# Kernel optimization log

Measured on AMD Instinct MI355X. Metric: run time of the kernel, lower is better.

Reference implementation:

```python
import jax, jax.numpy as jnp
import numpy as np

B_, K_, C_, HID_, T_, H_, W_ = 4, 4096, 384, 1536, 8, 32, 32
L_ = T_ * H_ * W_


def setup_inputs() -> dict:
    key = jax.random.key(0)
    ks = jax.random.split(key, 8)
    x_sparse = jax.random.normal(ks[0], (B_, K_, C_), dtype=jnp.float32)
    # unique, sorted per-batch active-token indices in [0, L)
    perm_keys = jax.random.split(ks[1], B_)
    indices = jax.vmap(lambda k: jnp.sort(jax.random.permutation(k, L_)[:K_]))(perm_keys).astype(jnp.int32)
    std = 0.02
    w1 = jax.random.normal(ks[2], (HID_, C_), dtype=jnp.float32) * std
    b1 = jnp.zeros((HID_,), dtype=jnp.float32)
    dw_w = jax.random.normal(ks[3], (HID_, 1, 3, 3), dtype=jnp.float32) * std  # depthwise OIHW, I=1
    dw_b = jnp.zeros((HID_,), dtype=jnp.float32)
    w2 = jax.random.normal(ks[4], (C_, HID_), dtype=jnp.float32) * std
    b2 = jnp.zeros((C_,), dtype=jnp.float32)
    return {"x_sparse": x_sparse, "indices": indices, "B": B_, "L": L_, "H": H_, "W": W_,
            "w1": w1, "b1": b1, "dw_w": dw_w, "dw_b": dw_b, "w2": w2, "b2": b2}


def reference(x_sparse, indices, B, L, H, W, w1, b1, dw_w, dw_b, w2, b2):
    K = x_sparse.shape[1]
    HID = w1.shape[0]
    T = L // (H * W)
    # sparse fc1: [B,K,C] @ [C,HID]
    h = jnp.einsum('bkc,hc->bkh', x_sparse, w1) + b1
    # scatter active tokens into zero-initialized dense grid [B,L,HID]
    bidx = jnp.arange(B)[:, None]  # [B,1]
    dense = jnp.zeros((B, L, HID), dtype=h.dtype).at[bidx, indices].set(h)
    # dense depthwise 3x3 conv on [B*T, HID, H, W]
    xs = dense.reshape(B * T, H, W, HID).transpose(0, 3, 1, 2)
    xs = jax.lax.conv_general_dilated(
        xs, dw_w, window_strides=(1, 1), padding='SAME',
        feature_group_count=HID,
        dimension_numbers=('NCHW', 'OIHW', 'NCHW')) + dw_b[None, :, None, None]
    flat = xs.transpose(0, 2, 3, 1).reshape(B, L, HID)
    # gather back the active tokens
    g = flat[bidx, indices]  # [B,K,HID]
    g = jax.nn.gelu(g, approximate=False)  # torch nn.GELU default is exact erf
    # sparse fc2: [B,K,HID] @ [HID,C_out]
    out = jnp.einsum('bkh,ch->bkc', g, w2) + b2
    return out
```

## Files before the change

### kernel.cpp

```cpp
#include <hip/hip_runtime.h>
#include <stdint.h>

using u16 = unsigned short;
using u32 = unsigned int;
using f32x4 = __attribute__((ext_vector_type(4))) float;
using s16x8 = __attribute__((ext_vector_type(8))) short;

#define DEVINL __device__ __forceinline__

constexpr int B_ = 4, K_ = 4096, C_ = 384, HID_ = 1536, H_ = 32, W_ = 32, L_ = 8192;
constexpr int M_ = B_ * K_;

DEVINL u16 f2bf(float f) {
    u32 u = __builtin_bit_cast(u32, f);
    u32 r = (u + 0x7FFFu + ((u >> 16) & 1u)) >> 16;
    return (u16)r;
}
DEVINL float bf2f(u16 h) {
    u32 u = ((u32)h) << 16;
    return __builtin_bit_cast(float, u);
}

template <int N>
DEVINL void wait_vmcnt() {
    asm volatile("s_waitcnt vmcnt(%0)" ::"n"(N) : "memory");
}

__global__ __launch_bounds__(256) void prep_kernel(
    const float* __restrict__ x, const float* __restrict__ w1, const float* __restrict__ w2,
    const float* __restrict__ dww, const int* __restrict__ indices,
    u16* __restrict__ xb, u16* __restrict__ w1b, u16* __restrict__ w2b,
    float* __restrict__ dwT, int* __restrict__ pos2k, u16* __restrict__ hzero) {
    const int i = blockIdx.x * 256 + threadIdx.x;
    if (i < 933888) {
        const float* src;
        u16* dst;
        if (i < 786432) { src = x + (size_t)i * 8; dst = xb + (size_t)i * 8; }
        else if (i < 860160) { src = w1 + (size_t)(i - 786432) * 8; dst = w1b + (size_t)(i - 786432) * 8; }
        else { src = w2 + (size_t)(i - 860160) * 8; dst = w2b + (size_t)(i - 860160) * 8; }
        float4 a = ((const float4*)src)[0];
        float4 b = ((const float4*)src)[1];
        s16x8 o;
        o[0] = (short)f2bf(a.x); o[1] = (short)f2bf(a.y);
        o[2] = (short)f2bf(a.z); o[3] = (short)f2bf(a.w);
        o[4] = (short)f2bf(b.x); o[5] = (short)f2bf(b.y);
        o[6] = (short)f2bf(b.z); o[7] = (short)f2bf(b.w);
        *(s16x8*)dst = o;
    } else if (i < 947712) {
        int t = i - 933888;
        int j = t / 1536;
        int hh = t - j * 1536;
        dwT[j * 1536 + hh] = dww[hh * 9 + j];
    } else if (i < 964096) {
        int t = i - 947712;
        int b = t >> 12;
        pos2k[(b << 13) + indices[t]] = t & 4095;
    } else if (i < 964288) {
        int t = i - 964096;
        s16x8 z = {0, 0, 0, 0, 0, 0, 0, 0};
        *(s16x8*)(hzero + t * 8) = z;
    }
}

template <int BM, int BN, int KDIM, bool OUT_BF16, int CB, int DEPTH>
__global__ __launch_bounds__(256) void gemm_pipe_kernel(
    const u16* __restrict__ A,
    const u16* __restrict__ Bt,
    const float* __restrict__ bias,
    void* __restrict__ Cv,
    int Ndim) {
    constexpr int BK = 32;
    constexpr int NSTEPS = KDIM / BK;
    static_assert(NSTEPS >= DEPTH, "");
    static_assert(DEPTH == 3 || DEPTH == 4, "");
    constexpr int ACH = BM / 16;
    constexpr int BCH = BN / 16;
    constexpr int CPW = (ACH + BCH) / 4;
    constexpr int ASZ = BM * BK;
    constexpr int BSZ = BN * BK;
    constexpr int FM = BM / 32;
    constexpr int FN = BN / 32;
    __shared__ u16 As[DEPTH * ASZ];
    __shared__ u16 Bs[DEPTH * BSZ];

    const int flat = blockIdx.x;
    const int per = gridDim.x >> 3;
    const int lid = (flat & 7) * per + (flat >> 3);
    const int rb = lid / CB;
    const int cb = lid - rb * CB;
    const int row0 = rb * BM;
    const int col0 = cb * BN;

    const int tid = threadIdx.x;
    const int wave = tid >> 6;
    const int lane = tid & 63;
    const int sr = lane >> 2;
    const int scw = (((lane & 3) ^ ((sr >> 1) & 3))) * 8;
    const int wr = (wave >> 1) * (FM * 16);
    const int wc = (wave & 1) * (FN * 16);
    const int fq = lane >> 4;
    const int fr = lane & 15;
    const int rchunk = fq ^ ((fr >> 1) & 3);

    f32x4 acc[FM][FN];
#pragma unroll
    for (int m = 0; m < FM; ++m)
#pragma unroll
        for (int n = 0; n < FN; ++n) acc[m][n] = f32x4{0.f, 0.f, 0.f, 0.f};

    const int c0ch = wave * CPW;

    auto stage = [&](int bi, int k0) {
#pragma unroll
        for (int q = 0; q < CPW; ++q) {
            const int c = c0ch + q;
            if (c < ACH) {
                const u16* g = A + (size_t)(row0 + c * 16 + sr) * KDIM + k0 + scw;
                __builtin_amdgcn_global_load_lds(
                    (const __attribute__((address_space(1))) void*)g,
                    (__attribute__((address_space(3))) void*)(As + bi * ASZ + c * 512), 16, 0, 0);
            } else {
                const int cc = c - ACH;
                const u16* g = Bt + (size_t)(col0 + cc * 16 + sr) * KDIM + k0 + scw;
                __builtin_amdgcn_global_load_lds(
                    (const __attribute__((address_space(1))) void*)g,
                    (__attribute__((address_space(3))) void*)(Bs + bi * BSZ + cc * 512), 16, 0, 0);
            }
        }
    };

    auto compute = [&](int bi) {
        s16x8 af[FM], bf_[FN];
#pragma unroll
        for (int m = 0; m < FM; ++m)
            af[m] = *(const s16x8*)(As + bi * ASZ + (wr + m * 16 + fr) * BK + rchunk * 8);
#pragma unroll
        for (int n = 0; n < FN; ++n)
            bf_[n] = *(const s16x8*)(Bs + bi * BSZ + (wc + n * 16 + fr) * BK + rchunk * 8);
        __builtin_amdgcn_s_setprio(1);
#pragma unroll
        for (int m = 0; m < FM; ++m)
#pragma unroll
            for (int n = 0; n < FN; ++n)
                acc[m][n] = __builtin_amdgcn_mfma_f32_16x16x32_bf16(af[m], bf_[n], acc[m][n], 0, 0, 0);
        __builtin_amdgcn_s_setprio(0);
    };

#pragma unroll
    for (int p = 0; p < DEPTH - 1; ++p) stage(p, p * BK);

    for (int i = 0; i < NSTEPS - (DEPTH - 1); ++i) {
        wait_vmcnt<(DEPTH - 2) * CPW>();
        __builtin_amdgcn_s_barrier();
        __builtin_amdgcn_sched_barrier(0);
        stage((i + DEPTH - 1) % DEPTH, (i + DEPTH - 1) * BK);
        compute(i % DEPTH);
    }
    if constexpr (DEPTH == 4) {
        wait_vmcnt<2 * CPW>();
        __builtin_amdgcn_s_barrier();
        __builtin_amdgcn_sched_barrier(0);
        compute((NSTEPS - 3) % DEPTH);
    }
    wait_vmcnt<CPW>();
    __builtin_amdgcn_s_barrier();
    __builtin_amdgcn_sched_barrier(0);
    compute((NSTEPS - 2) % DEPTH);
    wait_vmcnt<0>();
    __builtin_amdgcn_s_barrier();
    __builtin_amdgcn_sched_barrier(0);
    compute((NSTEPS - 1) % DEPTH);

#pragma unroll
    for (int n = 0; n < FN; ++n) {
        const int col = col0 + wc + n * 16 + fr;
        const float bv = bias[col];
#pragma unroll
        for (int m = 0; m < FM; ++m) {
            const int rowb = row0 + wr + m * 16 + fq * 4;
#pragma unroll
            for (int j = 0; j < 4; ++j) {
                float v = acc[m][n][j] + bv;
                if constexpr (OUT_BF16)
                    ((u16*)Cv)[(size_t)(rowb + j) * Ndim + col] = f2bf(v);
                else
                    ((float*)Cv)[(size_t)(rowb + j) * Ndim + col] = v;
            }
        }
    }
}

constexpr int TPB_CONV = 8;
__global__ __launch_bounds__(192) void conv_gelu_kernel(
    const u16* __restrict__ h,
    const int* __restrict__ indices,
    const int* __restrict__ pos2k,
    const float* __restrict__ dwT,
    const float* __restrict__ dwb,
    u16* __restrict__ g)
{
    __shared__ int nbr[TPB_CONV][9];

    const int flat = blockIdx.x;
    const int lb = (flat & 7) * ((M_ / TPB_CONV) >> 3) + (flat >> 3);
    const int tok0 = lb * TPB_CONV;
    const int tid = threadIdx.x;
    const int c0 = tid * 8;

    if (tid < TPB_CONV * 9) {
        const int t = tid / 9;
        const int j = tid - t * 9;
        const int token = tok0 + t;
        const int b = token >> 12;
        const int pos = indices[token];
        const int x = pos & 31;
        const int y = (pos >> 5) & 31;
        const int tb = pos & ~1023;
        const int dy = j / 3 - 1;
        const int dx = j - (j / 3) * 3 - 1;
        const int yy = y + dy;
        const int xx = x + dx;
        int row = M_;
        if (yy >= 0 && yy < 32 && xx >= 0 && xx < 32) {
            const int kp = pos2k[(b << 13) + tb + (yy << 5) + xx];
            if (kp >= 0) row = (b << 12) + kp;
        }
        nbr[t][j] = row;
    }

    f32x4 wv[9][2];
#pragma unroll
    for (int j = 0; j < 9; ++j) {
        wv[j][0] = *(const f32x4*)(dwT + j * 1536 + c0);
        wv[j][1] = *(const f32x4*)(dwT + j * 1536 + c0 + 4);
    }
    f32x4 bs0 = *(const f32x4*)(dwb + c0);
    f32x4 bs1 = *(const f32x4*)(dwb + c0 + 4);
#pragma unroll
    for (int j = 0; j < 9; ++j)
        asm volatile("" : "+v"(wv[j][0]), "+v"(wv[j][1]));
    asm volatile("" : "+v"(bs0), "+v"(bs1));
    __syncthreads();

#pragma unroll 1
    for (int ti = 0; ti < TPB_CONV; ++ti) {
        const int token = tok0 + ti;

        s16x8 hv[9];
#pragma unroll
        for (int j = 0; j < 9; ++j)
            hv[j] = *(const s16x8*)(h + (size_t)nbr[ti][j] * 1536 + c0);

        float acc[8];
#pragma unroll
        for (int q = 0; q < 4; ++q) { acc[q] = bs0[q]; acc[q + 4] = bs1[q]; }

#pragma unroll
        for (int j = 0; j < 9; ++j) {
#pragma unroll
            for (int q = 0; q < 8; ++q)
                acc[q] += bf2f((u16)hv[j][q]) * ((q < 4) ? wv[j][0][q] : wv[j][1][q - 4]);
        }

        s16x8 o;
#pragma unroll
        for (int q = 0; q < 8; ++q) {
            const float v = acc[q];
            const float xs = v * 0.70710678118654752f;
            const float x2 = xs * xs;
            const float er = 1.1283791670955126f * xs *
                (1.0f + x2 * (-0.333333333333f + x2 * (0.1f + x2 * (-0.023809523810f))));
            const float gl = 0.5f * v * (1.0f + er);
            o[q] = (short)f2bf(gl);
        }
        *(s16x8*)(g + (size_t)token * 1536 + c0) = o;
    }
}

extern "C" void kernel_launch(void* const* d_in, const int* in_sizes, int n_in,
                              void* d_out, int out_size, void* d_ws, size_t ws_size,
                              hipStream_t stream) {
    (void)in_sizes; (void)n_in; (void)out_size; (void)ws_size;
    const float* x   = (const float*)d_in[0];
    const int* indices = (const int*)d_in[1];
    const float* w1  = (const float*)d_in[6];
    const float* b1  = (const float*)d_in[7];
    const float* dww = (const float*)d_in[8];
    const float* dwb = (const float*)d_in[9];
    const float* w2  = (const float*)d_in[10];
    const float* b2  = (const float*)d_in[11];

    char* ws = (char*)d_ws;
    size_t off = 0;
    auto alloc = [&](size_t bytes) -> void* {
        void* p = ws + off;
        off += (bytes + 255) & ~(size_t)255;
        return p;
    };
    u16*   Abf   = (u16*)alloc((size_t)M_ * C_ * 2);
    u16*   W1b   = (u16*)alloc((size_t)HID_ * C_ * 2);
    u16*   W2b   = (u16*)alloc((size_t)C_ * HID_ * 2);
    float* dwT   = (float*)alloc((size_t)9 * HID_ * 4);
    int*   pos2k = (int*)alloc((size_t)B_ * L_ * 4);
    u16*   hbuf  = (u16*)alloc((size_t)(M_ + 1) * HID_ * 2);
    u16*   gbuf  = (u16*)alloc((size_t)M_ * HID_ * 2);

    hipMemsetAsync(pos2k, 0xFF, (size_t)B_ * L_ * 4, stream);
    prep_kernel<<<3767, 256, 0, stream>>>(x, w1, w2, dww, indices,
                                          Abf, W1b, W2b, dwT, pos2k,
                                          hbuf + (size_t)M_ * HID_);

    gemm_pipe_kernel<128, 128, C_, true, HID_ / 128, 3>
        <<<(M_ / 128) * (HID_ / 128), 256, 0, stream>>>(Abf, W1b, b1, hbuf, HID_);

    conv_gelu_kernel<<<M_ / TPB_CONV, 192, 0, stream>>>(hbuf, indices, pos2k, dwT, dwb, gbuf);

    gemm_pipe_kernel<128, 128, HID_, false, C_ / 128, 4>
        <<<(M_ / 128) * (C_ / 128), 256, 0, stream>>>(gbuf, W2b, b2, (float*)d_out, C_);
}
```

Measured before the change: 187.0 us.

## Replace GEMM kernel with 256x128 tile, 8-wave, double-buffered 64-K pipeline

Both GEMMs now use a new kernel with 256x128 output tiles, 512 threads (8 waves, each computing 64x64), and BK=64 split into two 32-wide halves with double buffering. Global-to-LDS loads for the next tile are interleaved between MFMA groups inside each half-step, with the LDS swizzle changed to match. The larger tile raises arithmetic intensity and cuts the grid size. In exchange it uses more accumulator registers per wave and leaves fewer blocks to spread across CUs, especially for the small-N fc2 GEMM.

```diff
diff --git a/kernel.cpp b/kernel.cpp
--- a/kernel.cpp
+++ b/kernel.cpp
@@ -7,6 +7,8 @@
 using s16x8 = __attribute__((ext_vector_type(8))) short;
 
 #define DEVINL __device__ __forceinline__
+#define AS1 __attribute__((address_space(1)))
+#define AS3 __attribute__((address_space(3)))
 
 constexpr int B_ = 4, K_ = 4096, C_ = 384, HID_ = 1536, H_ = 32, W_ = 32, L_ = 8192;
 constexpr int M_ = B_ * K_;
@@ -62,122 +64,137 @@
     }
 }
 
-template <int BM, int BN, int KDIM, bool OUT_BF16, int CB, int DEPTH>
-__global__ __launch_bounds__(256) void gemm_pipe_kernel(
+template <int KDIM, bool OUT_BF16, int CB>
+__global__ __launch_bounds__(512, 2) void gemm4p_kernel(
     const u16* __restrict__ A,
     const u16* __restrict__ Bt,
     const float* __restrict__ bias,
     void* __restrict__ Cv,
     int Ndim) {
-    constexpr int BK = 32;
-    constexpr int NSTEPS = KDIM / BK;
-    static_assert(NSTEPS >= DEPTH, "");
-    static_assert(DEPTH == 3 || DEPTH == 4, "");
-    constexpr int ACH = BM / 16;
-    constexpr int BCH = BN / 16;
-    constexpr int CPW = (ACH + BCH) / 4;
-    constexpr int ASZ = BM * BK;
-    constexpr int BSZ = BN * BK;
-    constexpr int FM = BM / 32;
-    constexpr int FN = BN / 32;
-    __shared__ u16 As[DEPTH * ASZ];
-    __shared__ u16 Bs[DEPTH * BSZ];
+    constexpr int NT = KDIM / 64;
+    static_assert(KDIM % 64 == 0 && NT >= 2, "");
+    __shared__ u16 As[2 * 2 * 256 * 32];
+    __shared__ u16 Bs[2 * 2 * 128 * 32];
 
     const int flat = blockIdx.x;
     const int per = gridDim.x >> 3;
     const int lid = (flat & 7) * per + (flat >> 3);
     const int rb = lid / CB;
     const int cb = lid - rb * CB;
-    const int row0 = rb * BM;
-    const int col0 = cb * BN;
+    const int row0 = rb * 256;
+    const int col0 = cb * 128;
 
     const int tid = threadIdx.x;
     const int wave = tid >> 6;
     const int lane = tid & 63;
-    const int sr = lane >> 2;
-    const int scw = (((lane & 3) ^ ((sr >> 1) & 3))) * 8;
-    const int wr = (wave >> 1) * (FM * 16);
-    const int wc = (wave & 1) * (FN * 16);
+    const int rl = (wave << 4) + (lane >> 2);
+    const int csw = (((lane & 3) ^ ((lane >> 2) & 3)) << 3);
+    const int wm = wave >> 1;
+    const int wn = wave & 1;
     const int fq = lane >> 4;
     const int fr = lane & 15;
-    const int rchunk = fq ^ ((fr >> 1) & 3);
-
-    f32x4 acc[FM][FN];
-#pragma unroll
-    for (int m = 0; m < FM; ++m)
-#pragma unroll
-        for (int n = 0; n < FN; ++n) acc[m][n] = f32x4{0.f, 0.f, 0.f, 0.f};
-
-    const int c0ch = wave * CPW;
-
-    auto stage = [&](int bi, int k0) {
-#pragma unroll
-        for (int q = 0; q < CPW; ++q) {
-            const int c = c0ch + q;
-            if (c < ACH) {
-                const u16* g = A + (size_t)(row0 + c * 16 + sr) * KDIM + k0 + scw;
-                __builtin_amdgcn_global_load_lds(
-                    (const __attribute__((address_space(1))) void*)g,
-                    (__attribute__((address_space(3))) void*)(As + bi * ASZ + c * 512), 16, 0, 0);
-            } else {
-                const int cc = c - ACH;
-                const u16* g = Bt + (size_t)(col0 + cc * 16 + sr) * KDIM + k0 + scw;
-                __builtin_amdgcn_global_load_lds(
-                    (const __attribute__((address_space(1))) void*)g,
-                    (__attribute__((address_space(3))) void*)(Bs + bi * BSZ + cc * 512), 16, 0, 0);
-            }
-        }
-    };
-
-    auto compute = [&](int bi) {
-        s16x8 af[FM], bf_[FN];
-#pragma unroll
-        for (int m = 0; m < FM; ++m)
-            af[m] = *(const s16x8*)(As + bi * ASZ + (wr + m * 16 + fr) * BK + rchunk * 8);
-#pragma unroll
-        for (int n = 0; n < FN; ++n)
-            bf_[n] = *(const s16x8*)(Bs + bi * BSZ + (wc + n * 16 + fr) * BK + rchunk * 8);
+    const int ksw = ((fq ^ (fr & 3)) << 3);
+
+    auto stA = [&](int buf, int kh, int kt) {
+#pragma unroll
+        for (int i = 0; i < 2; ++i) {
+            const u16* g = A + (size_t)(row0 + (i << 7) + rl) * KDIM + kt * 64 + kh * 32 + csw;
+            __builtin_amdgcn_global_load_lds(
+                (const AS1 void*)g,
+                (AS3 void*)(As + ((buf * 2 + kh) * 256 + (i << 7) + (wave << 4)) * 32), 16, 0, 0);
+        }
+    };
+    auto stB = [&](int buf, int kh, int kt) {
+        const u16* g = Bt + (size_t)(col0 + rl) * KDIM + kt * 64 + kh * 32 + csw;
+        __builtin_amdgcn_global_load_lds(
+            (const AS1 void*)g,
+            (AS3 void*)(Bs + ((buf * 2 + kh) * 128 + (wave << 4)) * 32), 16, 0, 0);
+    };
+    auto ldA = [&](int buf, int ks, int m) {
+        return *(const s16x8*)(As + ((buf * 2 + ks) * 256 + wm * 64 + m * 16 + fr) * 32 + ksw);
+    };
+    auto ldB = [&](int buf, int ks, int n) {
+        return *(const s16x8*)(Bs + ((buf * 2 + ks) * 128 + wn * 64 + n * 16 + fr) * 32 + ksw);
+    };
+
+    f32x4 acc[4][4];
+#pragma unroll
+    for (int m = 0; m < 4; ++m)
+#pragma unroll
+        for (int n = 0; n < 4; ++n) acc[m][n] = f32x4{0.f, 0.f, 0.f, 0.f};
+
+    stA(0, 0, 0); stB(0, 0, 0); stA(0, 1, 0); stB(0, 1, 0);
+    wait_vmcnt<3>();
+    __builtin_amdgcn_s_barrier();
+
+    for (int t = 0; t < NT; ++t) {
+        const int buf = t & 1;
+        const int nb = buf ^ 1;
+        const bool st = (t + 1 < NT);
+        s16x8 a0, a1, a2, a3, bfr[4];
+
+        a0 = ldA(buf, 0, 0); a1 = ldA(buf, 0, 1);
+#pragma unroll
+        for (int n = 0; n < 4; ++n) bfr[n] = ldB(buf, 0, n);
+        if (st) stA(nb, 0, t + 1);
         __builtin_amdgcn_s_setprio(1);
 #pragma unroll
-        for (int m = 0; m < FM; ++m)
-#pragma unroll
-            for (int n = 0; n < FN; ++n)
-                acc[m][n] = __builtin_amdgcn_mfma_f32_16x16x32_bf16(af[m], bf_[n], acc[m][n], 0, 0, 0);
+        for (int n = 0; n < 4; ++n)
+            acc[0][n] = __builtin_amdgcn_mfma_f32_16x16x32_bf16(a0, bfr[n], acc[0][n], 0, 0, 0);
+#pragma unroll
+        for (int n = 0; n < 4; ++n)
+            acc[1][n] = __builtin_amdgcn_mfma_f32_16x16x32_bf16(a1, bfr[n], acc[1][n], 0, 0, 0);
         __builtin_amdgcn_s_setprio(0);
-    };
-
-#pragma unroll
-    for (int p = 0; p < DEPTH - 1; ++p) stage(p, p * BK);
-
-    for (int i = 0; i < NSTEPS - (DEPTH - 1); ++i) {
-        wait_vmcnt<(DEPTH - 2) * CPW>();
+
+        a2 = ldA(buf, 0, 2); a3 = ldA(buf, 0, 3);
+        if (st) stB(nb, 0, t + 1);
+        __builtin_amdgcn_s_setprio(1);
+#pragma unroll
+        for (int n = 0; n < 4; ++n)
+            acc[2][n] = __builtin_amdgcn_mfma_f32_16x16x32_bf16(a2, bfr[n], acc[2][n], 0, 0, 0);
+#pragma unroll
+        for (int n = 0; n < 4; ++n)
+            acc[3][n] = __builtin_amdgcn_mfma_f32_16x16x32_bf16(a3, bfr[n], acc[3][n], 0, 0, 0);
+        __builtin_amdgcn_s_setprio(0);
+        if (st) wait_vmcnt<3>(); else wait_vmcnt<0>();
         __builtin_amdgcn_s_barrier();
-        __builtin_amdgcn_sched_barrier(0);
-        stage((i + DEPTH - 1) % DEPTH, (i + DEPTH - 1) * BK);
-        compute(i % DEPTH);
-    }
-    if constexpr (DEPTH == 4) {
-        wait_vmcnt<2 * CPW>();
-        __builtin_amdgcn_s_barrier();
-        __builtin_amdgcn_sched_barrier(0);
-        compute((NSTEPS - 3) % DEPTH);
-    }
-    wait_vmcnt<CPW>();
-    __builtin_amdgcn_s_barrier();
-    __builtin_amdgcn_sched_barrier(0);
-    compute((NSTEPS - 2) % DEPTH);
-    wait_vmcnt<0>();
-    __builtin_amdgcn_s_barrier();
-    __builtin_amdgcn_sched_barrier(0);
-    compute((NSTEPS - 1) % DEPTH);
-
-#pragma unroll
-    for (int n = 0; n < FN; ++n) {
-        const int col = col0 + wc + n * 16 + fr;
+
+        a0 = ldA(buf, 1, 0); a1 = ldA(buf, 1, 1);
+#pragma unroll
+        for (int n = 0; n < 4; ++n) bfr[n] = ldB(buf, 1, n);
+        if (st) stA(nb, 1, t + 1);
+        __builtin_amdgcn_s_setprio(1);
+#pragma unroll
+        for (int n = 0; n < 4; ++n)
+            acc[0][n] = __builtin_amdgcn_mfma_f32_16x16x32_bf16(a0, bfr[n], acc[0][n], 0, 0, 0);
+#pragma unroll
+        for (int n = 0; n < 4; ++n)
+            acc[1][n] = __builtin_amdgcn_mfma_f32_16x16x32_bf16(a1, bfr[n], acc[1][n], 0, 0, 0);
+        __builtin_amdgcn_s_setprio(0);
+
+        a2 = ldA(buf, 1, 2); a3 = ldA(buf, 1, 3);
+        if (st) stB(nb, 1, t + 1);
+        __builtin_amdgcn_s_setprio(1);
+#pragma unroll
+        for (int n = 0; n < 4; ++n)
+            acc[2][n] = __builtin_amdgcn_mfma_f32_16x16x32_bf16(a2, bfr[n], acc[2][n], 0, 0, 0);
+#pragma unroll
+        for (int n = 0; n < 4; ++n)
+            acc[3][n] = __builtin_amdgcn_mfma_f32_16x16x32_bf16(a3, bfr[n], acc[3][n], 0, 0, 0);
+        __builtin_amdgcn_s_setprio(0);
+        if (st) {
+            wait_vmcnt<3>();
+            __builtin_amdgcn_s_barrier();
+        }
+    }
+
+#pragma unroll
+    for (int n = 0; n < 4; ++n) {
+        const int col = col0 + wn * 64 + n * 16 + fr;
         const float bv = bias[col];
 #pragma unroll
-        for (int m = 0; m < FM; ++m) {
-            const int rowb = row0 + wr + m * 16 + fq * 4;
+        for (int m = 0; m < 4; ++m) {
+            const int rowb = row0 + wm * 64 + m * 16 + fq * 4;
 #pragma unroll
             for (int j = 0; j < 4; ++j) {
                 float v = acc[m][n][j] + bv;
@@ -310,11 +327,11 @@
                                           Abf, W1b, W2b, dwT, pos2k,
                                           hbuf + (size_t)M_ * HID_);
 
-    gemm_pipe_kernel<128, 128, C_, true, HID_ / 128, 3>
-        <<<(M_ / 128) * (HID_ / 128), 256, 0, stream>>>(Abf, W1b, b1, hbuf, HID_);
+    gemm4p_kernel<C_, true, HID_ / 128>
+        <<<(M_ / 256) * (HID_ / 128), 512, 0, stream>>>(Abf, W1b, b1, hbuf, HID_);
 
     conv_gelu_kernel<<<M_ / TPB_CONV, 192, 0, stream>>>(hbuf, indices, pos2k, dwT, dwb, gbuf);
 
-    gemm_pipe_kernel<128, 128, HID_, false, C_ / 128, 4>
-        <<<(M_ / 128) * (C_ / 128), 256, 0, stream>>>(gbuf, W2b, b2, (float*)d_out, C_);
-}
+    gemm4p_kernel<HID_, false, C_ / 128>
+        <<<(M_ / 256) * (C_ / 128), 512, 0, stream>>>(gbuf, W2b, b2, (float*)d_out, C_);
+}
```

Measured after the change: 197.0 us. 5.3% more time.
